# Optimization experiments

Measured on AMD Instinct MI355X. Metric: run time of the kernel, lower is better.

## Reference

```python
import jax, jax.numpy as jnp
import numpy as np

N_TOPICS = 256
BATCH = 131072


def setup_inputs() -> dict:
    key = jax.random.key(0)
    k = jax.random.split(key, 6)
    n, b = N_TOPICS, BATCH
    s = 1.0 / np.sqrt(n)  # matches torch RNNCell uniform(-1/sqrt(h), 1/sqrt(h)) scale
    return {
        "z": jax.random.normal(k[0], (b, n), jnp.float32),
        "h0": jax.random.uniform(k[1], (1, n), jnp.float32),
        "W_ih": jax.random.uniform(k[2], (n, n), jnp.float32, -s, s),
        "W_hh": jax.random.uniform(k[3], (n, n), jnp.float32, -s, s),
        "b_ih": jax.random.uniform(k[4], (n,), jnp.float32, -s, s),
        "b_hh": jax.random.uniform(k[5], (n,), jnp.float32, -s, s),
    }


def _stick_breaking(x):
    # torch.distributions.StickBreakingTransform._call
    D = x.shape[-1]
    offset = jnp.arange(D, 0, -1, dtype=x.dtype)          # [D, D-1, ..., 1]
    zc = jax.nn.sigmoid(x - jnp.log(offset))
    fi = jnp.finfo(x.dtype)
    zc = jnp.clip(zc, fi.tiny, 1.0 - fi.eps)              # _clipped_sigmoid
    z_cumprod = jnp.cumprod(1.0 - zc, axis=-1)
    ones = jnp.ones(x.shape[:-1] + (1,), x.dtype)
    return jnp.concatenate([zc, ones], -1) * jnp.concatenate([ones, z_cumprod], -1)


def reference(z, h0, W_ih, W_hh, b_ih, b_hh):
    n = W_ih.shape[0]
    D = n - 1
    b = b_ih + b_hh
    # step 0: rnncell(h0) with zero hidden state -> tanh(h0 @ W_ih.T + b_ih + b_hh)
    h1 = jnp.tanh(h0 @ W_ih.T + b)                        # (1, n)
    # steps i>0: rnncell(h, h) = tanh(h @ (W_ih + W_hh).T + b_ih + b_hh)
    Wc = (W_ih + W_hh).T

    def step(h, _):
        hn = jnp.tanh(h @ Wc + b)
        return hn, hn

    _, hs = jax.lax.scan(step, h1, None, length=D - 1)    # (D-1, 1, n)
    H = jnp.concatenate([h1[None], hs], axis=0)[:, 0, :]  # (D, n)
    eta = jax.nn.sigmoid(H @ z.T).T                       # (batch, D)
    return _stick_breaking(eta)                           # (batch, n)
```

## Files before the change

### kernel.cpp

```cpp
#include <hip/hip_runtime.h>

#define NTOP 256

typedef __attribute__((ext_vector_type(8))) short bf16x8;
typedef __attribute__((ext_vector_type(4))) float f32x4;

__device__ inline unsigned int packbf(float x) {
  unsigned int u = __float_as_uint(x);
  unsigned int r = (u + 0x7fffu + ((u >> 16) & 1u)) & 0xffff0000u;
  float res = x - __uint_as_float(r);
  unsigned int u2 = __float_as_uint(res);
  unsigned int r2 = u2 + 0x7fffu + ((u2 >> 16) & 1u);
  return r | (r2 >> 16);
}

__device__ inline float tanh_fast(float x) {
  float e = __expf(2.f * x);
  return 1.f - 2.f / (e + 1.f);
}

template <int CTRL>
__device__ inline float dpp_f(float v) {
  return __int_as_float(__builtin_amdgcn_update_dpp(
      0, __float_as_int(v), CTRL, 0xf, 0xf, true));
}

__global__ __launch_bounds__(1024)
__attribute__((amdgpu_waves_per_eu(4, 4)))
void rsbc_recur(
    const float* __restrict__ Wih, const float* __restrict__ Whh,
    const float* __restrict__ bih, const float* __restrict__ bhh,
    const float* __restrict__ h0, unsigned int* __restrict__ Hpack) {
  __shared__ float hA[4][68], hB[4][68];
  const int tid = threadIdx.x;
  const int j = tid >> 2, qt = tid & 3, k0 = qt * 64;
  const float bj = bih[j] + bhh[j];

  float4 w[16];
  {
    const float4* wp = reinterpret_cast<const float4*>(Wih + j * NTOP + k0);
#pragma unroll
    for (int q = 0; q < 16; ++q) w[q] = wp[q];
  }
  if (tid < NTOP) hA[tid >> 6][tid & 63] = h0[tid];
  __syncthreads();

  {
    const float* hq = hA[qt];
    float a0 = 0.f, a1 = 0.f, a2 = 0.f, a3 = 0.f;
#pragma unroll
    for (int q = 0; q < 16; ++q) {
      float4 hv = *reinterpret_cast<const float4*>(hq + 4 * q);
      a0 = fmaf(hv.x, w[q].x, a0);
      a1 = fmaf(hv.y, w[q].y, a1);
      a2 = fmaf(hv.z, w[q].z, a2);
      a3 = fmaf(hv.w, w[q].w, a3);
    }
    float sv = (a0 + a1) + (a2 + a3);
    sv += dpp_f<0xB1>(sv);
    sv += dpp_f<0x4E>(sv);
    if (qt == 0) {
      float v = tanh_fast(sv + bj);
      hB[j >> 6][j & 63] = v;
      Hpack[j] = packbf(v);
    }
  }
  {
    const float4* wq = reinterpret_cast<const float4*>(Whh + j * NTOP + k0);
#pragma unroll
    for (int q = 0; q < 16; ++q) {
      float4 t = wq[q];
      w[q].x += t.x; w[q].y += t.y; w[q].z += t.z; w[q].w += t.w;
    }
  }
  __syncthreads();

#pragma unroll 1
  for (int s = 1; s < 255; ++s) {
    const float(*hr)[68] = (s & 1) ? hB : hA;
    float(*hw)[68] = (s & 1) ? hA : hB;
    const float* hq = hr[qt];
    float a0 = 0.f, a1 = 0.f, a2 = 0.f, a3 = 0.f;
#pragma unroll
    for (int q = 0; q < 16; ++q) {
      float4 hv = *reinterpret_cast<const float4*>(hq + 4 * q);
      a0 = fmaf(hv.x, w[q].x, a0);
      a1 = fmaf(hv.y, w[q].y, a1);
      a2 = fmaf(hv.z, w[q].z, a2);
      a3 = fmaf(hv.w, w[q].w, a3);
    }
    float sv = (a0 + a1) + (a2 + a3);
    sv += dpp_f<0xB1>(sv);
    sv += dpp_f<0x4E>(sv);
    if (qt == 0) {
      float v = tanh_fast(sv + bj);
      hw[j >> 6][j & 63] = v;
      Hpack[s * NTOP + j] = packbf(v);
    }
    __syncthreads();
  }
}

__global__ __launch_bounds__(512)
__attribute__((amdgpu_waves_per_eu(2, 2)))
void rsbc_gemm_sb(
    const float* __restrict__ z, const unsigned int* __restrict__ Hpack,
    float* __restrict__ out) {
  constexpr int AS = 72;
  constexpr int BS = 72;
  constexpr int ES = 260;
  __shared__ __align__(16) char smem[135168];
  __shared__ float logtab[256];
  ushort* Ahi = reinterpret_cast<ushort*>(smem);
  ushort* Alo = Ahi + 128 * AS;
  ushort* Bhi = Alo + 128 * AS;
  ushort* Blo = Bhi + 256 * BS;
  float* eta = reinterpret_cast<float*>(smem);
  float* segT = eta + 128 * ES;

  const int tid = threadIdx.x;
  const size_t row0 = (size_t)blockIdx.x * 128;
  const int wid = tid >> 6, lane = tid & 63;
  const int wr = wid >> 2, wc = wid & 3;
  const int l15 = lane & 15, l4 = lane >> 4;

  if (tid < 255) logtab[tid] = logf((float)(255 - tid));

  f32x4 acc[4][4];
#pragma unroll
  for (int mt = 0; mt < 4; ++mt)
#pragma unroll
    for (int nt = 0; nt < 4; ++nt) acc[mt][nt] = (f32x4){0.f, 0.f, 0.f, 0.f};

  for (int kc = 0; kc < 4; ++kc) {
    const int kb = kc * 64;
    float4 zreg[4];
#pragma unroll
    for (int it = 0; it < 4; ++it) {
      int idx = tid + 512 * it;
      int r = idx >> 4, q = idx & 15;
      zreg[it] = *reinterpret_cast<const float4*>(
          z + (row0 + r) * NTOP + kb + 4 * q);
    }
    uint4 hreg[8];
#pragma unroll
    for (int it = 0; it < 8; ++it) {
      int idx = tid + 512 * it;
      int r = idx >> 4, q = idx & 15;
      hreg[it] = (r < 255)
                     ? *reinterpret_cast<const uint4*>(
                           Hpack + r * NTOP + kb + 4 * q)
                     : make_uint4(0u, 0u, 0u, 0u);
    }
    __syncthreads();
#pragma unroll
    for (int it = 0; it < 4; ++it) {
      int idx = tid + 512 * it;
      int r = idx >> 4, q = idx & 15;
      float4 v = zreg[it];
      unsigned int p0 = packbf(v.x), p1 = packbf(v.y),
                   p2 = packbf(v.z), p3 = packbf(v.w);
      *reinterpret_cast<ushort4*>(&Ahi[r * AS + 4 * q]) = make_ushort4(
          (ushort)(p0 >> 16), (ushort)(p1 >> 16),
          (ushort)(p2 >> 16), (ushort)(p3 >> 16));
      *reinterpret_cast<ushort4*>(&Alo[r * AS + 4 * q]) = make_ushort4(
          (ushort)(p0 & 0xffff), (ushort)(p1 & 0xffff),
          (ushort)(p2 & 0xffff), (ushort)(p3 & 0xffff));
    }
#pragma unroll
    for (int it = 0; it < 8; ++it) {
      int idx = tid + 512 * it;
      int r = idx >> 4, q = idx & 15;
      uint4 hv = hreg[it];
      *reinterpret_cast<ushort4*>(&Bhi[r * BS + 4 * q]) = make_ushort4(
          (ushort)(hv.x >> 16), (ushort)(hv.y >> 16),
          (ushort)(hv.z >> 16), (ushort)(hv.w >> 16));
      *reinterpret_cast<ushort4*>(&Blo[r * BS + 4 * q]) = make_ushort4(
          (ushort)(hv.x & 0xffff), (ushort)(hv.y & 0xffff),
          (ushort)(hv.z & 0xffff), (ushort)(hv.w & 0xffff));
    }
    __syncthreads();
#pragma unroll
    for (int ks = 0; ks < 2; ++ks) {
      const int ko = ks * 32 + l4 * 8;
      bf16x8 afh[4], afl[4], bfh[4], bfl[4];
#pragma unroll
      for (int mt = 0; mt < 4; ++mt) {
        int r = 64 * wr + 16 * mt + l15;
        afh[mt] = *reinterpret_cast<const bf16x8*>(&Ahi[r * AS + ko]);
        afl[mt] = *reinterpret_cast<const bf16x8*>(&Alo[r * AS + ko]);
      }
#pragma unroll
      for (int nt = 0; nt < 4; ++nt) {
        int n = 64 * wc + 16 * nt + l15;
        bfh[nt] = *reinterpret_cast<const bf16x8*>(&Bhi[n * BS + ko]);
        bfl[nt] = *reinterpret_cast<const bf16x8*>(&Blo[n * BS + ko]);
      }
#pragma unroll
      for (int mt = 0; mt < 4; ++mt)
#pragma unroll
        for (int nt = 0; nt < 4; ++nt) {
          acc[mt][nt] = __builtin_amdgcn_mfma_f32_16x16x32_bf16(
              afh[mt], bfh[nt], acc[mt][nt], 0, 0, 0);
          acc[mt][nt] = __builtin_amdgcn_mfma_f32_16x16x32_bf16(
              afh[mt], bfl[nt], acc[mt][nt], 0, 0, 0);
          acc[mt][nt] = __builtin_amdgcn_mfma_f32_16x16x32_bf16(
              afl[mt], bfh[nt], acc[mt][nt], 0, 0, 0);
        }
    }
  }
  __syncthreads();

#pragma unroll
  for (int mt = 0; mt < 4; ++mt) {
    int rbase = 64 * wr + 16 * mt + 4 * l4;
#pragma unroll
    for (int nt = 0; nt < 4; ++nt) {
      int c = 64 * wc + 16 * nt + l15;
#pragma unroll
      for (int i = 0; i < 4; ++i) {
        float x = acc[mt][nt][i];
        eta[(rbase + i) * ES + c] = 1.f / (1.f + __expf(-x));
      }
    }
  }
  __syncthreads();

  const int r = tid >> 2, qk = tid & 3;
  const int kbeg = 64 * qk, kend = (qk == 3) ? 255 : 64 * qk + 64;
  float* er = &eta[r * ES];
  {
    float cp = 1.f;
#pragma unroll 4
    for (int k = kbeg; k < kend; ++k) {
      float x = er[k] - logtab[k];
      float zc = 1.f / (1.f + __expf(-x));
      zc = fminf(fmaxf(zc, 1.1754943508222875e-38f), 0.99999988079071045f);
      er[k] = zc * cp;
      cp *= 1.f - zc;
    }
    segT[r * 4 + qk] = cp;
  }
  __syncthreads();
  {
    float p = 1.f;
    if (qk > 0) p *= segT[r * 4 + 0];
    if (qk > 1) p *= segT[r * 4 + 1];
    if (qk > 2) p *= segT[r * 4 + 2];
    if (qk > 0) {
#pragma unroll 4
      for (int k = kbeg; k < kend; ++k) er[k] *= p;
    }
    if (qk == 3) er[255] = p * segT[r * 4 + 3];
  }
  __syncthreads();

#pragma unroll
  for (int it = 0; it < 16; ++it) {
    int idx = tid + 512 * it;
    int rr = idx >> 6, cq = idx & 63;
    float4 vv = *reinterpret_cast<const float4*>(&eta[rr * ES + 4 * cq]);
    *reinterpret_cast<float4*>(&out[(row0 + rr) * NTOP + 4 * cq]) = vv;
  }
}

extern "C" void kernel_launch(void* const* d_in, const int* in_sizes, int n_in,
                              void* d_out, int out_size, void* d_ws, size_t ws_size,
                              hipStream_t stream) {
  const float* z   = (const float*)d_in[0];
  const float* h0  = (const float*)d_in[1];
  const float* Wih = (const float*)d_in[2];
  const float* Whh = (const float*)d_in[3];
  const float* bih = (const float*)d_in[4];
  const float* bhh = (const float*)d_in[5];
  float* out = (float*)d_out;
  unsigned int* Hpack = (unsigned int*)d_ws;

  rsbc_recur<<<1, 1024, 0, stream>>>(Wih, Whh, bih, bhh, h0, Hpack);
  const int nrows = out_size / NTOP;
  const int blocks = nrows / 128;
  rsbc_gemm_sb<<<blocks, 512, 0, stream>>>(z, Hpack, out);
}
```

Before: 323.2 us.

## Run the RNN recurrence on split-bf16 MFMA and batch hidden-state stores

The serial recurrence kernel now does each step's 256x256 matvec with bf16 MFMA 16x16x32 instructions. Weights and the hidden state are split into hi/lo bf16 pairs to keep near-fp32 accuracy. Each wave owns 16 output rows, and the DPP cross-lane reduction is gone. Hidden-state outputs are buffered in a 32-step shared-memory history and flushed to global memory in bulk, which takes per-step global stores off the latency-critical loop. The cost is four MFMAs per K-chunk in dependent chains, which could lengthen each step if MFMA latency dominates.

```diff
diff --git a/kernel.cpp b/kernel.cpp
--- a/kernel.cpp
+++ b/kernel.cpp
@@ -19,85 +19,112 @@
   return 1.f - 2.f / (e + 1.f);
 }
 
-template <int CTRL>
-__device__ inline float dpp_f(float v) {
-  return __int_as_float(__builtin_amdgcn_update_dpp(
-      0, __float_as_int(v), CTRL, 0xf, 0xf, true));
-}
-
 __global__ __launch_bounds__(1024)
 __attribute__((amdgpu_waves_per_eu(4, 4)))
 void rsbc_recur(
     const float* __restrict__ Wih, const float* __restrict__ Whh,
     const float* __restrict__ bih, const float* __restrict__ bhh,
     const float* __restrict__ h0, unsigned int* __restrict__ Hpack) {
-  __shared__ float hA[4][68], hB[4][68];
+  __shared__ ushort hh[2][NTOP];
+  __shared__ ushort hl[2][NTOP];
+  __shared__ unsigned int hist[32][NTOP];
   const int tid = threadIdx.x;
-  const int j = tid >> 2, qt = tid & 3, k0 = qt * 64;
+  const int w = tid >> 6, l = tid & 63;
+  const int l15 = l & 15, g = l >> 4;
+  const int j = 16 * w + l15;
   const float bj = bih[j] + bhh[j];
 
-  float4 w[16];
-  {
-    const float4* wp = reinterpret_cast<const float4*>(Wih + j * NTOP + k0);
-#pragma unroll
-    for (int q = 0; q < 16; ++q) w[q] = wp[q];
-  }
-  if (tid < NTOP) hA[tid >> 6][tid & 63] = h0[tid];
-  __syncthreads();
-
-  {
-    const float* hq = hA[qt];
-    float a0 = 0.f, a1 = 0.f, a2 = 0.f, a3 = 0.f;
-#pragma unroll
-    for (int q = 0; q < 16; ++q) {
-      float4 hv = *reinterpret_cast<const float4*>(hq + 4 * q);
-      a0 = fmaf(hv.x, w[q].x, a0);
-      a1 = fmaf(hv.y, w[q].y, a1);
-      a2 = fmaf(hv.z, w[q].z, a2);
-      a3 = fmaf(hv.w, w[q].w, a3);
-    }
-    float sv = (a0 + a1) + (a2 + a3);
-    sv += dpp_f<0xB1>(sv);
-    sv += dpp_f<0x4E>(sv);
-    if (qt == 0) {
-      float v = tanh_fast(sv + bj);
-      hB[j >> 6][j & 63] = v;
-      Hpack[j] = packbf(v);
-    }
-  }
-  {
-    const float4* wq = reinterpret_cast<const float4*>(Whh + j * NTOP + k0);
-#pragma unroll
-    for (int q = 0; q < 16; ++q) {
-      float4 t = wq[q];
-      w[q].x += t.x; w[q].y += t.y; w[q].z += t.z; w[q].w += t.w;
-    }
-  }
-  __syncthreads();
+  if (tid < NTOP) {
+    unsigned int u = packbf(h0[tid]);
+    hh[0][tid] = (ushort)(u >> 16);
+    hl[0][tid] = (ushort)(u & 0xffffu);
+  }
+
+  bf16x8 bh[8], bl[8];
+#pragma unroll
+  for (int t = 0; t < 8; ++t) {
+    const float* src = Wih + j * NTOP + 32 * t + 8 * g;
+    float4 u0 = *reinterpret_cast<const float4*>(src);
+    float4 u1 = *reinterpret_cast<const float4*>(src + 4);
+    float f[8] = {u0.x, u0.y, u0.z, u0.w, u1.x, u1.y, u1.z, u1.w};
+#pragma unroll
+    for (int e = 0; e < 8; ++e) {
+      unsigned int p = packbf(f[e]);
+      bh[t][e] = (short)(p >> 16);
+      bl[t][e] = (short)(p & 0xffffu);
+    }
+  }
+  __syncthreads();
+
+  auto step = [&](int rb, int wb, int r) {
+    const ushort* Hh = hh[rb];
+    const ushort* Hl = hl[rb];
+    f32x4 acc0 = {0.f, 0.f, 0.f, 0.f}, acc1 = {0.f, 0.f, 0.f, 0.f};
+#pragma unroll
+    for (int t = 0; t < 8; t += 2) {
+      bf16x8 a0h = *reinterpret_cast<const bf16x8*>(Hh + 32 * t + 8 * g);
+      bf16x8 a0l = *reinterpret_cast<const bf16x8*>(Hl + 32 * t + 8 * g);
+      acc0 = __builtin_amdgcn_mfma_f32_16x16x32_bf16(a0h, bh[t], acc0, 0, 0, 0);
+      acc0 = __builtin_amdgcn_mfma_f32_16x16x32_bf16(a0h, bl[t], acc0, 0, 0, 0);
+      acc0 = __builtin_amdgcn_mfma_f32_16x16x32_bf16(a0l, bh[t], acc0, 0, 0, 0);
+      acc0 = __builtin_amdgcn_mfma_f32_16x16x32_bf16(a0l, bl[t], acc0, 0, 0, 0);
+      bf16x8 a1h = *reinterpret_cast<const bf16x8*>(Hh + 32 * (t + 1) + 8 * g);
+      bf16x8 a1l = *reinterpret_cast<const bf16x8*>(Hl + 32 * (t + 1) + 8 * g);
+      acc1 = __builtin_amdgcn_mfma_f32_16x16x32_bf16(a1h, bh[t + 1], acc1, 0, 0, 0);
+      acc1 = __builtin_amdgcn_mfma_f32_16x16x32_bf16(a1h, bl[t + 1], acc1, 0, 0, 0);
+      acc1 = __builtin_amdgcn_mfma_f32_16x16x32_bf16(a1l, bh[t + 1], acc1, 0, 0, 0);
+      acc1 = __builtin_amdgcn_mfma_f32_16x16x32_bf16(a1l, bl[t + 1], acc1, 0, 0, 0);
+    }
+    float d = acc0[0] + acc1[0];
+    float v = tanh_fast(d + bj);
+    unsigned int u = packbf(v);
+    if (g == 0) {
+      hh[wb][j] = (ushort)(u >> 16);
+      hl[wb][j] = (ushort)(u & 0xffffu);
+      hist[r & 31][j] = u;
+    }
+    __syncthreads();
+  };
+
+  step(0, 1, 0);
+
+#pragma unroll
+  for (int t = 0; t < 8; ++t) {
+    const float* s1 = Wih + j * NTOP + 32 * t + 8 * g;
+    const float* s2 = Whh + j * NTOP + 32 * t + 8 * g;
+    float4 a0 = *reinterpret_cast<const float4*>(s1);
+    float4 a1 = *reinterpret_cast<const float4*>(s1 + 4);
+    float4 c0 = *reinterpret_cast<const float4*>(s2);
+    float4 c1 = *reinterpret_cast<const float4*>(s2 + 4);
+    float f[8] = {a0.x + c0.x, a0.y + c0.y, a0.z + c0.z, a0.w + c0.w,
+                  a1.x + c1.x, a1.y + c1.y, a1.z + c1.z, a1.w + c1.w};
+#pragma unroll
+    for (int e = 0; e < 8; ++e) {
+      unsigned int p = packbf(f[e]);
+      bh[t][e] = (short)(p >> 16);
+      bl[t][e] = (short)(p & 0xffffu);
+    }
+  }
 
 #pragma unroll 1
-  for (int s = 1; s < 255; ++s) {
-    const float(*hr)[68] = (s & 1) ? hB : hA;
-    float(*hw)[68] = (s & 1) ? hA : hB;
-    const float* hq = hr[qt];
-    float a0 = 0.f, a1 = 0.f, a2 = 0.f, a3 = 0.f;
-#pragma unroll
-    for (int q = 0; q < 16; ++q) {
-      float4 hv = *reinterpret_cast<const float4*>(hq + 4 * q);
-      a0 = fmaf(hv.x, w[q].x, a0);
-      a1 = fmaf(hv.y, w[q].y, a1);
-      a2 = fmaf(hv.z, w[q].z, a2);
-      a3 = fmaf(hv.w, w[q].w, a3);
-    }
-    float sv = (a0 + a1) + (a2 + a3);
-    sv += dpp_f<0xB1>(sv);
-    sv += dpp_f<0x4E>(sv);
-    if (qt == 0) {
-      float v = tanh_fast(sv + bj);
-      hw[j >> 6][j & 63] = v;
-      Hpack[s * NTOP + j] = packbf(v);
-    }
-    __syncthreads();
+  for (int r = 1; r < 255; ++r) {
+    step(r & 1, (r + 1) & 1, r);
+    if ((r & 31) == 31) {
+      const int r0 = r - 31;
+#pragma unroll
+      for (int it = 0; it < 8; ++it) {
+        int idx = tid + 1024 * it;
+        int sr = idx >> 8, jj = idx & 255;
+        Hpack[(r0 + sr) * NTOP + jj] = hist[sr][jj];
+      }
+      __syncthreads();
+    }
+  }
+#pragma unroll
+  for (int it = 0; it < 8; ++it) {
+    int idx = tid + 1024 * it;
+    int sr = idx >> 8, jj = idx & 255;
+    if (sr < 31) Hpack[(224 + sr) * NTOP + jj] = hist[sr][jj];
   }
 }
 
```

Measured after the change: 466.4 us. +44.3%, slower.

## Restructure serial RNN recurrence to 512 threads with 8 outputs per lane group

Applied to the files above, without the earlier changes.

The single-block recurrence kernel now uses 512 threads (8 waves instead of 16). Each 16-lane group computes 8 output rows, holding those weight rows in registers and reducing across lanes with four DPP steps. The packed bf16 writes of H are moved off the per-step critical path: each step writes the previous step's hidden vector from shared memory. The intent is to cut barrier cost and per-step latency in the 254-step serial loop, at the price of more register pressure and a longer reduction chain per lane.

```diff
diff --git a/kernel.cpp b/kernel.cpp
--- a/kernel.cpp
+++ b/kernel.cpp
@@ -25,80 +25,89 @@
       0, __float_as_int(v), CTRL, 0xf, 0xf, true));
 }
 
-__global__ __launch_bounds__(1024)
-__attribute__((amdgpu_waves_per_eu(4, 4)))
+__device__ inline float red16(float v) {
+  v += dpp_f<0xB1>(v);
+  v += dpp_f<0x4E>(v);
+  v += dpp_f<0x114>(v);
+  v += dpp_f<0x118>(v);
+  return v;
+}
+
+__global__ __launch_bounds__(512)
+__attribute__((amdgpu_waves_per_eu(2, 2)))
 void rsbc_recur(
     const float* __restrict__ Wih, const float* __restrict__ Whh,
     const float* __restrict__ bih, const float* __restrict__ bhh,
     const float* __restrict__ h0, unsigned int* __restrict__ Hpack) {
-  __shared__ float hA[4][68], hB[4][68];
+  __shared__ float hbuf[2][NTOP];
   const int tid = threadIdx.x;
-  const int j = tid >> 2, qt = tid & 3, k0 = qt * 64;
-  const float bj = bih[j] + bhh[j];
-
-  float4 w[16];
-  {
-    const float4* wp = reinterpret_cast<const float4*>(Wih + j * NTOP + k0);
-#pragma unroll
-    for (int q = 0; q < 16; ++q) w[q] = wp[q];
-  }
-  if (tid < NTOP) hA[tid >> 6][tid & 63] = h0[tid];
-  __syncthreads();
-
-  {
-    const float* hq = hA[qt];
-    float a0 = 0.f, a1 = 0.f, a2 = 0.f, a3 = 0.f;
-#pragma unroll
-    for (int q = 0; q < 16; ++q) {
-      float4 hv = *reinterpret_cast<const float4*>(hq + 4 * q);
-      a0 = fmaf(hv.x, w[q].x, a0);
-      a1 = fmaf(hv.y, w[q].y, a1);
-      a2 = fmaf(hv.z, w[q].z, a2);
-      a3 = fmaf(hv.w, w[q].w, a3);
-    }
-    float sv = (a0 + a1) + (a2 + a3);
-    sv += dpp_f<0xB1>(sv);
-    sv += dpp_f<0x4E>(sv);
-    if (qt == 0) {
-      float v = tanh_fast(sv + bj);
-      hB[j >> 6][j & 63] = v;
-      Hpack[j] = packbf(v);
-    }
-  }
-  {
-    const float4* wq = reinterpret_cast<const float4*>(Whh + j * NTOP + k0);
-#pragma unroll
-    for (int q = 0; q < 16; ++q) {
-      float4 t = wq[q];
-      w[q].x += t.x; w[q].y += t.y; w[q].z += t.z; w[q].w += t.w;
-    }
-  }
+  const int w = tid >> 6, l = tid & 63;
+  const int r16 = l >> 4, l15 = l & 15;
+  const int R = w * 4 + r16;
+  const int j0 = R * 8;
+  const int kcol = 4 * l15;
+
+  float bb[8];
+#pragma unroll
+  for (int jj = 0; jj < 8; ++jj) bb[jj] = bih[j0 + jj] + bhh[j0 + jj];
+
+  float4 wt[8][4];
+#pragma unroll
+  for (int jj = 0; jj < 8; ++jj)
+#pragma unroll
+    for (int i = 0; i < 4; ++i)
+      wt[jj][i] = *reinterpret_cast<const float4*>(
+          Wih + (j0 + jj) * NTOP + 64 * i + kcol);
+
+  if (tid < NTOP) hbuf[0][tid] = h0[tid];
+  __syncthreads();
+
+  auto step = [&](const float* hr, float* hw) {
+    float4 h4[4];
+#pragma unroll
+    for (int i = 0; i < 4; ++i)
+      h4[i] = *reinterpret_cast<const float4*>(hr + 64 * i + kcol);
+    float a[8];
+#pragma unroll
+    for (int jj = 0; jj < 8; ++jj) {
+      float t = 0.f;
+#pragma unroll
+      for (int i = 0; i < 4; ++i) {
+        t = fmaf(h4[i].x, wt[jj][i].x, t);
+        t = fmaf(h4[i].y, wt[jj][i].y, t);
+        t = fmaf(h4[i].z, wt[jj][i].z, t);
+        t = fmaf(h4[i].w, wt[jj][i].w, t);
+      }
+      a[jj] = red16(t);
+    }
+    if (l15 == 15) {
+#pragma unroll
+      for (int jj = 0; jj < 8; ++jj)
+        hw[j0 + jj] = tanh_fast(a[jj] + bb[jj]);
+    }
+  };
+
+  step(hbuf[0], hbuf[1]);
+#pragma unroll
+  for (int jj = 0; jj < 8; ++jj)
+#pragma unroll
+    for (int i = 0; i < 4; ++i) {
+      float4 t = *reinterpret_cast<const float4*>(
+          Whh + (j0 + jj) * NTOP + 64 * i + kcol);
+      wt[jj][i].x += t.x; wt[jj][i].y += t.y;
+      wt[jj][i].z += t.z; wt[jj][i].w += t.w;
+    }
   __syncthreads();
 
 #pragma unroll 1
   for (int s = 1; s < 255; ++s) {
-    const float(*hr)[68] = (s & 1) ? hB : hA;
-    float(*hw)[68] = (s & 1) ? hA : hB;
-    const float* hq = hr[qt];
-    float a0 = 0.f, a1 = 0.f, a2 = 0.f, a3 = 0.f;
-#pragma unroll
-    for (int q = 0; q < 16; ++q) {
-      float4 hv = *reinterpret_cast<const float4*>(hq + 4 * q);
-      a0 = fmaf(hv.x, w[q].x, a0);
-      a1 = fmaf(hv.y, w[q].y, a1);
-      a2 = fmaf(hv.z, w[q].z, a2);
-      a3 = fmaf(hv.w, w[q].w, a3);
-    }
-    float sv = (a0 + a1) + (a2 + a3);
-    sv += dpp_f<0xB1>(sv);
-    sv += dpp_f<0x4E>(sv);
-    if (qt == 0) {
-      float v = tanh_fast(sv + bj);
-      hw[j >> 6][j & 63] = v;
-      Hpack[s * NTOP + j] = packbf(v);
-    }
+    const float* hr = hbuf[s & 1];
+    float* hw = hbuf[(s + 1) & 1];
+    if (tid < NTOP) Hpack[(s - 1) * NTOP + tid] = packbf(hr[tid]);
+    step(hr, hw);
     __syncthreads();
   }
+  if (tid < NTOP) Hpack[254 * NTOP + tid] = packbf(hbuf[1][tid]);
 }
 
 __global__ __launch_bounds__(512)
@@ -276,7 +285,7 @@
   float* out = (float*)d_out;
   unsigned int* Hpack = (unsigned int*)d_ws;
 
-  rsbc_recur<<<1, 1024, 0, stream>>>(Wih, Whh, bih, bhh, h0, Hpack);
+  rsbc_recur<<<1, 512, 0, stream>>>(Wih, Whh, bih, bhh, h0, Hpack);
   const int nrows = out_size / NTOP;
   const int blocks = nrows / 128;
   rsbc_gemm_sb<<<blocks, 512, 0, stream>>>(z, Hpack, out);
```

Result: slower. 525.0 us (+62.4%).
